# Kernel optimization log

Measured on AMD Instinct MI355X. Metric: run time of the kernel, lower is better.

Reference implementation:

```python
import jax, jax.numpy as jnp
import numpy as np

INV_SQRT2 = 0.7071067811865476
SCALES = 3


def dwt_analysis(x, dec_lo, dec_hi, scales):
    """Multi-level 1D DWT along last axis (pywt/ptwt convention).
    x: [B, D]. dec_lo/dec_hi are cross-correlation filters (torch conv1d
    semantics, i.e. the flipped pywt decomposition filters as stored by the
    repo). Returns [cA_s | cD_s | ... | cD_1] truncated to the last D columns
    (identity for Haar on power-of-two D)."""
    flen = dec_lo.shape[0]
    pad = (2 * flen - 3) // 2  # ptwt zero-pad; 0 for Haar (flen=2)
    filt = jnp.stack([dec_lo, dec_hi])[:, None, :]  # [2, 1, flen]
    lo = x[:, None, :]  # [B, 1, D]
    highs = []
    for _ in range(scales):
        out = jax.lax.conv_general_dilated(
            lo, filt, window_strides=(2,), padding=[(pad, pad)],
            dimension_numbers=('NCH', 'OIH', 'NCH'))  # [B, 2, D/2]
        lo = out[:, 0:1, :]
        highs.append(out[:, 1, :])
    coeffs = jnp.concatenate([lo[:, 0, :]] + highs[::-1], axis=-1)
    return coeffs[:, -x.shape[-1]:]


def setup_inputs() -> dict:
    key = jax.random.key(0)
    k1, k2, k3, k4, k5 = jax.random.split(key, 5)
    B, D = 4096, 4096
    x = jax.random.normal(k1, (B, D), jnp.float32)
    diag_s = jax.random.normal(k2, (D,), jnp.float32)
    diag_g = jax.random.normal(k3, (D,), jnp.float32)
    diag_b = jax.random.normal(k4, (D,), jnp.float32)
    perm = jax.random.permutation(k5, jnp.arange(D))  # random column permutation
    # Haar analysis filters in cross-correlation (torch conv1d) orientation
    dec_lo = jnp.array([INV_SQRT2, INV_SQRT2], jnp.float32)
    dec_hi = jnp.array([INV_SQRT2, -INV_SQRT2], jnp.float32)
    return {"x": x, "diag_s": diag_s, "diag_g": diag_g, "diag_b": diag_b,
            "dec_lo": dec_lo, "dec_hi": dec_hi, "perm": perm, "scales": SCALES}


def reference(x, diag_s, diag_g, diag_b, dec_lo, dec_hi, perm, scales):
    # mul_b: x @ diag(b) == columnwise scale (same math, no O(d^2) matmul)
    h = x * diag_b
    h = dwt_analysis(h, dec_lo, dec_hi, scales)
    # mul_p: x @ P for a permutation matrix == column gather
    h = jnp.take(h, perm, axis=1)
    h = h * diag_g  # mul_g
    h = dwt_analysis(h, dec_lo, dec_hi, scales)
    return h * diag_s  # mul_s
```

## Files before the change

### kernel.cpp

```cpp
#include <hip/hip_runtime.h>


#define D   4096
#define NT  256
#define R   2

#define C_INV_SQRT2 0.70710678118654752440f

typedef float vf2 __attribute__((ext_vector_type(2)));
typedef float vf4 __attribute__((ext_vector_type(4)));

static __device__ __forceinline__ int swz(int i) {
    return i ^ ((i >> 5) & 31);
}

static __device__ __forceinline__ void dwt3_reg(const float v[16],
                                                float a3[2], float d3[2],
                                                float d2[4], float d1[8]) {
    float a1[8];
    #pragma unroll
    for (int j = 0; j < 8; ++j) {
        a1[j] = (v[2 * j] + v[2 * j + 1]) * C_INV_SQRT2;
        d1[j] = (v[2 * j] - v[2 * j + 1]) * C_INV_SQRT2;
    }
    float a2[4];
    #pragma unroll
    for (int j = 0; j < 4; ++j) {
        a2[j] = (a1[2 * j] + a1[2 * j + 1]) * C_INV_SQRT2;
        d2[j] = (a1[2 * j] - a1[2 * j + 1]) * C_INV_SQRT2;
    }
    #pragma unroll
    for (int j = 0; j < 2; ++j) {
        a3[j] = (a2[2 * j] + a2[2 * j + 1]) * C_INV_SQRT2;
        d3[j] = (a2[2 * j] - a2[2 * j + 1]) * C_INV_SQRT2;
    }
}

__global__ __launch_bounds__(NT) void wavelet_rows_kernel(
    const float* __restrict__ x,
    const float* __restrict__ diag_s,
    const float* __restrict__ diag_g,
    const float* __restrict__ diag_b,
    const int*   __restrict__ perm,
    float*       __restrict__ out)
{
    __shared__ float buf[D];

    const int t = threadIdx.x;
    const size_t row0 = (size_t)blockIdx.x * R;

    float db[16], dg[16];
    int   pidx[16];
    {
        const vf4* b4 = (const vf4*)diag_b;
        const vf4* g4 = (const vf4*)diag_g;
        const int4* p4 = (const int4*)perm;
        #pragma unroll
        for (int k = 0; k < 4; ++k) {
            vf4 bv = b4[4 * t + k];
            db[4 * k + 0] = bv.x; db[4 * k + 1] = bv.y;
            db[4 * k + 2] = bv.z; db[4 * k + 3] = bv.w;
            vf4 gv = g4[4 * t + k];
            dg[4 * k + 0] = gv.x; dg[4 * k + 1] = gv.y;
            dg[4 * k + 2] = gv.z; dg[4 * k + 3] = gv.w;
            int4 pv = p4[4 * t + k];
            pidx[4 * k + 0] = pv.x; pidx[4 * k + 1] = pv.y;
            pidx[4 * k + 2] = pv.z; pidx[4 * k + 3] = pv.w;
        }
    }
    vf2 sA, sD3;
    vf4 sD2, sD1a, sD1b;
    {
        const vf2* s2 = (const vf2*)diag_s;
        const vf4* s4 = (const vf4*)diag_s;
        sA   = s2[t];
        sD3  = s2[256 + t];
        sD2  = s4[256 + t];
        sD1a = s4[512 + 2 * t];
        sD1b = s4[512 + 2 * t + 1];
    }

    for (int r = 0; r < R; ++r) {
        const vf4* x4 = (const vf4*)(x + (row0 + r) * (size_t)D);

        float v[16];
        #pragma unroll
        for (int k = 0; k < 4; ++k) {
            vf4 xv = x4[4 * t + k];
            v[4 * k + 0] = xv.x * db[4 * k + 0];
            v[4 * k + 1] = xv.y * db[4 * k + 1];
            v[4 * k + 2] = xv.z * db[4 * k + 2];
            v[4 * k + 3] = xv.w * db[4 * k + 3];
        }

        float a3[2], d3[2], d2[4], d1[8];
        dwt3_reg(v, a3, d3, d2, d1);

        #pragma unroll
        for (int j = 0; j < 2; ++j) buf[swz(2 * t + j)]        = a3[j];
        #pragma unroll
        for (int j = 0; j < 2; ++j) buf[swz(512 + 2 * t + j)]  = d3[j];
        #pragma unroll
        for (int j = 0; j < 4; ++j) buf[swz(1024 + 4 * t + j)] = d2[j];
        #pragma unroll
        for (int j = 0; j < 8; ++j) buf[swz(2048 + 8 * t + j)] = d1[j];

        __syncthreads();

        float w[16];
        #pragma unroll
        for (int k = 0; k < 16; ++k) {
            w[k] = buf[swz(pidx[k])] * dg[k];
        }

        if (r + 1 < R) __syncthreads();

        float b3[2], e3[2], e2[4], e1[8];
        dwt3_reg(w, b3, e3, e2, e1);

        float* orow = out + (row0 + r) * (size_t)D;
        {
            vf2* o2 = (vf2*)orow;
            vf2 ov;
            ov.x = b3[0] * sA.x;  ov.y = b3[1] * sA.y;
            __builtin_nontemporal_store(ov, &o2[t]);
            ov.x = e3[0] * sD3.x; ov.y = e3[1] * sD3.y;
            __builtin_nontemporal_store(ov, &o2[256 + t]);

            vf4* o4 = (vf4*)orow;
            vf4 o;
            o.x = e2[0] * sD2.x; o.y = e2[1] * sD2.y;
            o.z = e2[2] * sD2.z; o.w = e2[3] * sD2.w;
            __builtin_nontemporal_store(o, &o4[256 + t]);
            o.x = e1[0] * sD1a.x; o.y = e1[1] * sD1a.y;
            o.z = e1[2] * sD1a.z; o.w = e1[3] * sD1a.w;
            __builtin_nontemporal_store(o, &o4[512 + 2 * t]);
            o.x = e1[4] * sD1b.x; o.y = e1[5] * sD1b.y;
            o.z = e1[6] * sD1b.z; o.w = e1[7] * sD1b.w;
            __builtin_nontemporal_store(o, &o4[512 + 2 * t + 1]);
        }
    }
}

extern "C" void kernel_launch(void* const* d_in, const int* in_sizes, int n_in,
                              void* d_out, int out_size, void* d_ws, size_t ws_size,
                              hipStream_t stream) {
    const float* x      = (const float*)d_in[0];
    const float* diag_s = (const float*)d_in[1];
    const float* diag_g = (const float*)d_in[2];
    const float* diag_b = (const float*)d_in[3];
    const int* perm     = (const int*)d_in[6];
    float* out          = (float*)d_out;

    const int B = 4096 / R;
    wavelet_rows_kernel<<<B, NT, 0, stream>>>(x, diag_s, diag_g, diag_b, perm, out);
}
```

Before: 126.8 us.

## Interleave row chunks across threads and finish DWT level three with lane shuffles

Each thread now processes four strided 4-element chunks (index 256*k+t) instead of 16 contiguous elements. The third Haar level is completed by exchanging partial averages between neighbouring lanes with __shfl_xor. This makes global loads, LDS writes and output stores fully coalesced and sequential, so the XOR swizzle on shared memory is no longer needed. In exchange it adds shuffle instructions and divergent-looking odd/even selects, and output stores become narrower (scalar and vf2 instead of vf4).

New measurement: 126.0 us. About the same (-0.6%).

```diff
diff --git a/kernel.cpp b/kernel.cpp
--- a/kernel.cpp
+++ b/kernel.cpp
@@ -10,30 +10,18 @@
 typedef float vf2 __attribute__((ext_vector_type(2)));
 typedef float vf4 __attribute__((ext_vector_type(4)));
 
-static __device__ __forceinline__ int swz(int i) {
-    return i ^ ((i >> 5) & 31);
-}
-
-static __device__ __forceinline__ void dwt3_reg(const float v[16],
-                                                float a3[2], float d3[2],
-                                                float d2[4], float d1[8]) {
-    float a1[8];
-    #pragma unroll
-    for (int j = 0; j < 8; ++j) {
-        a1[j] = (v[2 * j] + v[2 * j + 1]) * C_INV_SQRT2;
-        d1[j] = (v[2 * j] - v[2 * j + 1]) * C_INV_SQRT2;
-    }
-    float a2[4];
-    #pragma unroll
-    for (int j = 0; j < 4; ++j) {
-        a2[j] = (a1[2 * j] + a1[2 * j + 1]) * C_INV_SQRT2;
-        d2[j] = (a1[2 * j] - a1[2 * j + 1]) * C_INV_SQRT2;
-    }
-    #pragma unroll
-    for (int j = 0; j < 2; ++j) {
-        a3[j] = (a2[2 * j] + a2[2 * j + 1]) * C_INV_SQRT2;
-        d3[j] = (a2[2 * j] - a2[2 * j + 1]) * C_INV_SQRT2;
-    }
+static __device__ __forceinline__ void haar_chunk(
+    float v0, float v1, float v2, float v3, int odd,
+    float& d1a, float& d1b, float& d2v, float& l3)
+{
+    float a10 = (v0 + v1) * C_INV_SQRT2;
+    d1a       = (v0 - v1) * C_INV_SQRT2;
+    float a11 = (v2 + v3) * C_INV_SQRT2;
+    d1b       = (v2 - v3) * C_INV_SQRT2;
+    float a2  = (a10 + a11) * C_INV_SQRT2;
+    d2v       = (a10 - a11) * C_INV_SQRT2;
+    float a2p = __shfl_xor(a2, 1);
+    l3 = (odd ? (a2p - a2) : (a2 + a2p)) * C_INV_SQRT2;
 }
 
 __global__ __launch_bounds__(NT) void wavelet_rows_kernel(
@@ -46,99 +34,68 @@
 {
     __shared__ float buf[D];
 
-    const int t = threadIdx.x;
+    const int t   = threadIdx.x;
+    const int s   = t >> 1;
+    const int odd = t & 1;
     const size_t row0 = (size_t)blockIdx.x * R;
 
-    float db[16], dg[16];
-    int   pidx[16];
+    vf4  db[4], dg[4];
+    int4 pidx[4];
+    vf2  sd1[4];
+    float sd2[4], sl3[4];
     {
         const vf4* b4 = (const vf4*)diag_b;
         const vf4* g4 = (const vf4*)diag_g;
         const int4* p4 = (const int4*)perm;
+        const vf2* s2 = (const vf2*)diag_s;
         #pragma unroll
         for (int k = 0; k < 4; ++k) {
-            vf4 bv = b4[4 * t + k];
-            db[4 * k + 0] = bv.x; db[4 * k + 1] = bv.y;
-            db[4 * k + 2] = bv.z; db[4 * k + 3] = bv.w;
-            vf4 gv = g4[4 * t + k];
-            dg[4 * k + 0] = gv.x; dg[4 * k + 1] = gv.y;
-            dg[4 * k + 2] = gv.z; dg[4 * k + 3] = gv.w;
-            int4 pv = p4[4 * t + k];
-            pidx[4 * k + 0] = pv.x; pidx[4 * k + 1] = pv.y;
-            pidx[4 * k + 2] = pv.z; pidx[4 * k + 3] = pv.w;
+            db[k]   = b4[256 * k + t];
+            dg[k]   = g4[256 * k + t];
+            pidx[k] = p4[256 * k + t];
+            sd1[k]  = s2[1024 + 256 * k + t];
+            sd2[k]  = diag_s[1024 + 256 * k + t];
+            sl3[k]  = diag_s[(odd ? 512 : 0) + 128 * k + s];
         }
-    }
-    vf2 sA, sD3;
-    vf4 sD2, sD1a, sD1b;
-    {
-        const vf2* s2 = (const vf2*)diag_s;
-        const vf4* s4 = (const vf4*)diag_s;
-        sA   = s2[t];
-        sD3  = s2[256 + t];
-        sD2  = s4[256 + t];
-        sD1a = s4[512 + 2 * t];
-        sD1b = s4[512 + 2 * t + 1];
     }
 
     for (int r = 0; r < R; ++r) {
         const vf4* x4 = (const vf4*)(x + (row0 + r) * (size_t)D);
 
-        float v[16];
         #pragma unroll
         for (int k = 0; k < 4; ++k) {
-            vf4 xv = x4[4 * t + k];
-            v[4 * k + 0] = xv.x * db[4 * k + 0];
-            v[4 * k + 1] = xv.y * db[4 * k + 1];
-            v[4 * k + 2] = xv.z * db[4 * k + 2];
-            v[4 * k + 3] = xv.w * db[4 * k + 3];
+            vf4 xv = x4[256 * k + t];
+            float d1a, d1b, d2v, l3;
+            haar_chunk(xv.x * db[k].x, xv.y * db[k].y,
+                       xv.z * db[k].z, xv.w * db[k].w, odd,
+                       d1a, d1b, d2v, l3);
+            vf2 dp; dp.x = d1a; dp.y = d1b;
+            *(vf2*)&buf[2048 + 512 * k + 2 * t] = dp;
+            buf[1024 + 256 * k + t] = d2v;
+            buf[(odd ? 512 : 0) + 128 * k + s] = l3;
         }
-
-        float a3[2], d3[2], d2[4], d1[8];
-        dwt3_reg(v, a3, d3, d2, d1);
-
-        #pragma unroll
-        for (int j = 0; j < 2; ++j) buf[swz(2 * t + j)]        = a3[j];
-        #pragma unroll
-        for (int j = 0; j < 2; ++j) buf[swz(512 + 2 * t + j)]  = d3[j];
-        #pragma unroll
-        for (int j = 0; j < 4; ++j) buf[swz(1024 + 4 * t + j)] = d2[j];
-        #pragma unroll
-        for (int j = 0; j < 8; ++j) buf[swz(2048 + 8 * t + j)] = d1[j];
 
         __syncthreads();
 
-        float w[16];
+        float* orow = out + (row0 + r) * (size_t)D;
         #pragma unroll
-        for (int k = 0; k < 16; ++k) {
-            w[k] = buf[swz(pidx[k])] * dg[k];
+        for (int k = 0; k < 4; ++k) {
+            float w0 = buf[pidx[k].x] * dg[k].x;
+            float w1 = buf[pidx[k].y] * dg[k].y;
+            float w2 = buf[pidx[k].z] * dg[k].z;
+            float w3 = buf[pidx[k].w] * dg[k].w;
+            float e1a, e1b, e2v, f3;
+            haar_chunk(w0, w1, w2, w3, odd, e1a, e1b, e2v, f3);
+
+            vf2 ep; ep.x = e1a * sd1[k].x; ep.y = e1b * sd1[k].y;
+            __builtin_nontemporal_store(ep, &((vf2*)orow)[1024 + 256 * k + t]);
+            __builtin_nontemporal_store(e2v * sd2[k],
+                                        &orow[1024 + 256 * k + t]);
+            __builtin_nontemporal_store(f3 * sl3[k],
+                                        &orow[(odd ? 512 : 0) + 128 * k + s]);
         }
 
         if (r + 1 < R) __syncthreads();
-
-        float b3[2], e3[2], e2[4], e1[8];
-        dwt3_reg(w, b3, e3, e2, e1);
-
-        float* orow = out + (row0 + r) * (size_t)D;
-        {
-            vf2* o2 = (vf2*)orow;
-            vf2 ov;
-            ov.x = b3[0] * sA.x;  ov.y = b3[1] * sA.y;
-            __builtin_nontemporal_store(ov, &o2[t]);
-            ov.x = e3[0] * sD3.x; ov.y = e3[1] * sD3.y;
-            __builtin_nontemporal_store(ov, &o2[256 + t]);
-
-            vf4* o4 = (vf4*)orow;
-            vf4 o;
-            o.x = e2[0] * sD2.x; o.y = e2[1] * sD2.y;
-            o.z = e2[2] * sD2.z; o.w = e2[3] * sD2.w;
-            __builtin_nontemporal_store(o, &o4[256 + t]);
-            o.x = e1[0] * sD1a.x; o.y = e1[1] * sD1a.y;
-            o.z = e1[2] * sD1a.z; o.w = e1[3] * sD1a.w;
-            __builtin_nontemporal_store(o, &o4[512 + 2 * t]);
-            o.x = e1[4] * sD1b.x; o.y = e1[5] * sD1b.y;
-            o.z = e1[6] * sD1b.z; o.w = e1[7] * sD1b.w;
-            __builtin_nontemporal_store(o, &o4[512 + 2 * t + 1]);
-        }
     }
 }
 
```
